# Kernel optimization log

Hardware: AMD Instinct MI355X
Metric: run time of the kernel (lower is better)

## Reference

```python
import jax, jax.numpy as jnp
import numpy as np

G, D, W, IN_CH, OUT_CH = 16, 8, 64, 3, 4
SKIPS = (4,)
B, N = 1, 65536


def _ilayers():
    il = [IN_CH] + [W] * (D - 1)
    for i in SKIPS:
        il[i + 1] += IN_CH
    return il


def setup_inputs() -> dict:
    key = jax.random.key(0)
    ks = jax.random.split(key, 2 * D + 3)
    inp = {"x": jax.random.normal(ks[0], (B, G, N, IN_CH), jnp.float32)}
    il = _ilayers()
    ki = 1
    for i, ci in enumerate(il):
        s = 1.0 / np.sqrt(ci)
        inp[f"w{i}"] = jax.random.uniform(ks[ki], (G, W, ci), jnp.float32, -s, s); ki += 1
        inp[f"b{i}"] = jax.random.uniform(ks[ki], (G, W), jnp.float32, -s, s); ki += 1
    s = 1.0 / np.sqrt(W)
    inp["w_out"] = jax.random.uniform(ks[ki], (G, OUT_CH, W), jnp.float32, -s, s)
    inp["b_out"] = jax.random.uniform(ks[ki + 1], (G, OUT_CH), jnp.float32, -s, s)
    return inp


def _plinear(h, w, b):
    # per-group linear: h [B,G,N,Ci], w [G,Co,Ci], b [G,Co] -> [B,G,N,Co]
    return jnp.einsum('bgnc,goc->bgno', h, w) + b[None, :, None, :]


def reference(x, w0, b0, w1, b1, w2, b2, w3, b3, w4, b4, w5, b5, w6, b6, w7, b7, w_out, b_out):
    ws = [w0, w1, w2, w3, w4, w5, w6, w7]
    bs = [b0, b1, b2, b3, b4, b5, b6, b7]
    h = x
    for i in range(D):
        h = jax.nn.relu(_plinear(h, ws[i], bs[i]))
        if i in SKIPS:
            # parallel_concat([x, h], G): per-group channel concat
            h = jnp.concatenate([x, h], axis=-1)
    out = _plinear(h, w_out, b_out)  # identity final activation
    return out, h
```

## Files before the change

### kernel.cpp

```cpp
#include <hip/hip_runtime.h>
#include <hip/hip_bf16.h>


#define NG 16
#define NPTS 65536
#define NT 4

typedef __attribute__((ext_vector_type(8))) short bf16x8;
typedef __attribute__((ext_vector_type(4))) float f32x4;
typedef __attribute__((ext_vector_type(4))) int i32x4;

#define SLOT_ELEMS 4096
#define GROUP_ELEMS (10 * SLOT_ELEMS)
#define WBUF_ELEMS (NG * GROUP_ELEMS)

__device__ __forceinline__ unsigned short f2bf(float f) {
  unsigned u = __builtin_bit_cast(unsigned, f);
  u += 0x7FFFu + ((u >> 16) & 1u);
  return (unsigned short)(u >> 16);
}
__device__ __forceinline__ float bf2f(unsigned short h) {
  return __builtin_bit_cast(float, ((unsigned)h) << 16);
}
__device__ __forceinline__ unsigned pkbf(float a, float b) {
  __hip_bfloat162 t = __float22bfloat162_rn(make_float2(a, b));
  unsigned u;
  __builtin_memcpy(&u, &t, 4);
  return u;
}
__device__ __forceinline__ float lo2f(unsigned u) { return __builtin_bit_cast(float, u << 16); }
__device__ __forceinline__ float hi2f(unsigned u) { return __builtin_bit_cast(float, u & 0xFFFF0000u); }
__device__ __forceinline__ bf16x8 pack4(unsigned a, unsigned b, unsigned cc, unsigned d) {
  i32x4 t;
  t[0] = (int)a; t[1] = (int)b; t[2] = (int)cc; t[3] = (int)d;
  return __builtin_bit_cast(bf16x8, t);
}

__device__ __forceinline__ int sig(int k) {
  int kt = k >> 5, qq = (k >> 3) & 3, j = k & 7;
  return (kt * 2 + (j >> 2)) * 16 + qq * 4 + (j & 3);
}

__global__ __launch_bounds__(256) void prep_weights(
    const float* __restrict__ w0, const float* __restrict__ w1,
    const float* __restrict__ w2, const float* __restrict__ w3,
    const float* __restrict__ w4, const float* __restrict__ w5,
    const float* __restrict__ w6, const float* __restrict__ w7,
    const float* __restrict__ w_out,
    unsigned short* __restrict__ whi, unsigned short* __restrict__ wlo) {
  int idx = blockIdx.x * 256 + threadIdx.x;
  if (idx >= WBUF_ELEMS) return;
  int g = idx / GROUP_ELEMS;
  int rem = idx - g * GROUP_ELEMS;
  int slot = rem / SLOT_ELEMS;
  int rc = rem - slot * SLOT_ELEMS;
  int row = rc >> 6, col = rc & 63;
  int sc = sig(col);
  float v = 0.0f;
  switch (slot) {
    case 0: if (col < 3) v = w0[g * 192 + row * 3 + col]; break;
    case 1: v = w1[g * 4096 + row * 64 + sc]; break;
    case 2: v = w2[g * 4096 + row * 64 + sc]; break;
    case 3: v = w3[g * 4096 + row * 64 + sc]; break;
    case 4: v = w4[g * 4096 + row * 64 + sc]; break;
    case 5: v = w5[g * 4288 + row * 67 + 3 + sc]; break;
    case 6: v = w6[g * 4096 + row * 64 + sc]; break;
    case 7: v = w7[g * 4096 + row * 64 + sc]; break;
    case 8: if (col < 3) v = w5[g * 4288 + row * 67 + col]; break;
    case 9: if (row < 4) v = w_out[g * 256 + row * 64 + sc]; break;
  }
  unsigned short h = f2bf(v);
  whi[idx] = h;
  wlo[idx] = f2bf(v - bf2f(h));
}

__device__ __forceinline__ void zeroC(f32x4 (&C)[4][NT]) {
#pragma unroll
  for (int mt = 0; mt < 4; ++mt)
#pragma unroll
    for (int nt = 0; nt < NT; ++nt) {
      f32x4 z = {0.f, 0.f, 0.f, 0.f};
      C[mt][nt] = z;
    }
}

__device__ __forceinline__ void cvt_all(f32x4 (&C)[4][NT], const float4* __restrict__ bias4,
                                        int q, bf16x8 (&Bh)[NT][2], bf16x8 (&Bl)[NT][2]) {
  float4 bs[4];
#pragma unroll
  for (int mt = 0; mt < 4; ++mt) bs[mt] = bias4[mt * 4 + q];
#pragma unroll
  for (int nt = 0; nt < NT; ++nt) {
    float v[4][4];
#pragma unroll
    for (int mt = 0; mt < 4; ++mt) {
      f32x4 cc = C[mt][nt];
      float t0 = fmaxf(cc[0] + bs[mt].x, 0.f);
      float t1 = fmaxf(cc[1] + bs[mt].y, 0.f);
      float t2 = fmaxf(cc[2] + bs[mt].z, 0.f);
      float t3 = fmaxf(cc[3] + bs[mt].w, 0.f);
      v[mt][0] = t0; v[mt][1] = t1; v[mt][2] = t2; v[mt][3] = t3;
      cc[0] = t0; cc[1] = t1; cc[2] = t2; cc[3] = t3;
      C[mt][nt] = cc;
    }
#pragma unroll
    for (int kt = 0; kt < 2; ++kt) {
      const float* a = v[2 * kt];
      const float* b = v[2 * kt + 1];
      unsigned u0 = pkbf(a[0], a[1]), u1 = pkbf(a[2], a[3]);
      unsigned u2 = pkbf(b[0], b[1]), u3 = pkbf(b[2], b[3]);
      Bh[nt][kt] = pack4(u0, u1, u2, u3);
      unsigned l0 = pkbf(a[0] - lo2f(u0), a[1] - hi2f(u0));
      unsigned l1 = pkbf(a[2] - lo2f(u1), a[3] - hi2f(u1));
      unsigned l2 = pkbf(b[0] - lo2f(u2), b[1] - hi2f(u2));
      unsigned l3 = pkbf(b[2] - lo2f(u3), b[3] - hi2f(u3));
      Bl[nt][kt] = pack4(l0, l1, l2, l3);
    }
  }
}

__device__ __forceinline__ void dense(const unsigned short* __restrict__ wh,
                                      const unsigned short* __restrict__ wl,
                                      int q, int c,
                                      const bf16x8 (&Bh)[NT][2], const bf16x8 (&Bl)[NT][2],
                                      f32x4 (&C)[4][NT]) {
  bf16x8 Ah[4][2];
#pragma unroll
  for (int mt = 0; mt < 4; ++mt)
#pragma unroll
    for (int kt = 0; kt < 2; ++kt)
      Ah[mt][kt] = *(const bf16x8*)(wh + (mt * 16 + c) * 64 + kt * 32 + q * 8);

#pragma unroll
  for (int mt = 0; mt < 4; ++mt)
#pragma unroll
    for (int kt = 0; kt < 2; ++kt) {
#pragma unroll
      for (int nt = 0; nt < NT; ++nt)
        C[mt][nt] = __builtin_amdgcn_mfma_f32_16x16x32_bf16(Ah[mt][kt], Bh[nt][kt], C[mt][nt], 0, 0, 0);
#pragma unroll
      for (int nt = 0; nt < NT; ++nt)
        C[mt][nt] = __builtin_amdgcn_mfma_f32_16x16x32_bf16(Ah[mt][kt], Bl[nt][kt], C[mt][nt], 0, 0, 0);
    }

#pragma unroll
  for (int mt = 0; mt < 4; ++mt)
#pragma unroll
    for (int kt = 0; kt < 2; ++kt) {
      bf16x8 Al = *(const bf16x8*)(wl + (mt * 16 + c) * 64 + kt * 32 + q * 8);
#pragma unroll
      for (int nt = 0; nt < NT; ++nt)
        C[mt][nt] = __builtin_amdgcn_mfma_f32_16x16x32_bf16(Al, Bh[nt][kt], C[mt][nt], 0, 0, 0);
    }
}

__device__ __forceinline__ void xpart(const unsigned short* __restrict__ wh,
                                      const unsigned short* __restrict__ wl,
                                      int q, int c, const float (&xr)[NT][3], f32x4 (&C)[4][NT]) {
  bf16x8 Bxh[NT], Bxl[NT];
#pragma unroll
  for (int nt = 0; nt < NT; ++nt) {
    unsigned u0 = 0, u1 = 0, l0 = 0, l1 = 0;
    if (q == 0) {
      u0 = pkbf(xr[nt][0], xr[nt][1]);
      u1 = pkbf(xr[nt][2], 0.f);
      l0 = pkbf(xr[nt][0] - lo2f(u0), xr[nt][1] - hi2f(u0));
      l1 = pkbf(xr[nt][2] - lo2f(u1), 0.f);
    }
    Bxh[nt] = pack4(u0, u1, 0, 0);
    Bxl[nt] = pack4(l0, l1, 0, 0);
  }
#pragma unroll
  for (int mt = 0; mt < 4; ++mt) {
    bf16x8 Ah = *(const bf16x8*)(wh + (mt * 16 + c) * 64 + q * 8);
    bf16x8 Al = *(const bf16x8*)(wl + (mt * 16 + c) * 64 + q * 8);
#pragma unroll
    for (int nt = 0; nt < NT; ++nt) {
      C[mt][nt] = __builtin_amdgcn_mfma_f32_16x16x32_bf16(Ah, Bxh[nt], C[mt][nt], 0, 0, 0);
      C[mt][nt] = __builtin_amdgcn_mfma_f32_16x16x32_bf16(Ah, Bxl[nt], C[mt][nt], 0, 0, 0);
      C[mt][nt] = __builtin_amdgcn_mfma_f32_16x16x32_bf16(Al, Bxh[nt], C[mt][nt], 0, 0, 0);
    }
  }
}

__global__ __launch_bounds__(256, 2) void mlp_mfma_kernel(
    const float* __restrict__ x,
    const float* __restrict__ b0, const float* __restrict__ b1,
    const float* __restrict__ b2, const float* __restrict__ b3,
    const float* __restrict__ b4, const float* __restrict__ b5,
    const float* __restrict__ b6, const float* __restrict__ b7,
    const float* __restrict__ b_out,
    const unsigned short* __restrict__ whi, const unsigned short* __restrict__ wlo,
    float* __restrict__ out, float* __restrict__ hfinal) {
  const int g = blockIdx.y;
  const int lane = threadIdx.x & 63;
  const int wv = threadIdx.x >> 6;
  const int q = lane >> 4;
  const int c = lane & 15;
  const int n0 = blockIdx.x * (64 * 4) + wv * 64;

  const unsigned short* wgh = whi + (size_t)g * GROUP_ELEMS;
  const unsigned short* wgl = wlo + (size_t)g * GROUP_ELEMS;

  float xr[NT][3];
#pragma unroll
  for (int nt = 0; nt < NT; ++nt) {
    const float* xp = x + ((size_t)g * NPTS + n0 + nt * 16 + c) * 3;
    xr[nt][0] = xp[0]; xr[nt][1] = xp[1]; xr[nt][2] = xp[2];
  }

  f32x4 C[4][NT];
  bf16x8 Bh[NT][2], Bl[NT][2];

  zeroC(C);
  xpart(wgh + 0 * SLOT_ELEMS, wgl + 0 * SLOT_ELEMS, q, c, xr, C);
  cvt_all(C, (const float4*)(b0 + g * 64), q, Bh, Bl);

  zeroC(C); dense(wgh + 1 * SLOT_ELEMS, wgl + 1 * SLOT_ELEMS, q, c, Bh, Bl, C);
  cvt_all(C, (const float4*)(b1 + g * 64), q, Bh, Bl);
  zeroC(C); dense(wgh + 2 * SLOT_ELEMS, wgl + 2 * SLOT_ELEMS, q, c, Bh, Bl, C);
  cvt_all(C, (const float4*)(b2 + g * 64), q, Bh, Bl);
  zeroC(C); dense(wgh + 3 * SLOT_ELEMS, wgl + 3 * SLOT_ELEMS, q, c, Bh, Bl, C);
  cvt_all(C, (const float4*)(b3 + g * 64), q, Bh, Bl);
  zeroC(C); dense(wgh + 4 * SLOT_ELEMS, wgl + 4 * SLOT_ELEMS, q, c, Bh, Bl, C);
  cvt_all(C, (const float4*)(b4 + g * 64), q, Bh, Bl);

  zeroC(C);
  xpart(wgh + 8 * SLOT_ELEMS, wgl + 8 * SLOT_ELEMS, q, c, xr, C);
  dense(wgh + 5 * SLOT_ELEMS, wgl + 5 * SLOT_ELEMS, q, c, Bh, Bl, C);
  cvt_all(C, (const float4*)(b5 + g * 64), q, Bh, Bl);

  zeroC(C); dense(wgh + 6 * SLOT_ELEMS, wgl + 6 * SLOT_ELEMS, q, c, Bh, Bl, C);
  cvt_all(C, (const float4*)(b6 + g * 64), q, Bh, Bl);
  zeroC(C); dense(wgh + 7 * SLOT_ELEMS, wgl + 7 * SLOT_ELEMS, q, c, Bh, Bl, C);
  cvt_all(C, (const float4*)(b7 + g * 64), q, Bh, Bl);

#pragma unroll
  for (int mt = 0; mt < 4; ++mt) {
#pragma unroll
    for (int nt = 0; nt < NT; ++nt) {
      size_t ptg = (size_t)g * NPTS + n0 + nt * 16 + c;
      f32x4 v = C[mt][nt];
      *(float4*)(hfinal + ptg * 64 + mt * 16 + q * 4) = make_float4(v[0], v[1], v[2], v[3]);
    }
  }

  f32x4 Co[NT];
#pragma unroll
  for (int nt = 0; nt < NT; ++nt) {
    f32x4 z = {0.f, 0.f, 0.f, 0.f};
    Co[nt] = z;
  }
#pragma unroll
  for (int kt = 0; kt < 2; ++kt) {
    bf16x8 Ah = *(const bf16x8*)(wgh + 9 * SLOT_ELEMS + c * 64 + kt * 32 + q * 8);
    bf16x8 Al = *(const bf16x8*)(wgl + 9 * SLOT_ELEMS + c * 64 + kt * 32 + q * 8);
#pragma unroll
    for (int nt = 0; nt < NT; ++nt) {
      Co[nt] = __builtin_amdgcn_mfma_f32_16x16x32_bf16(Ah, Bh[nt][kt], Co[nt], 0, 0, 0);
      Co[nt] = __builtin_amdgcn_mfma_f32_16x16x32_bf16(Ah, Bl[nt][kt], Co[nt], 0, 0, 0);
      Co[nt] = __builtin_amdgcn_mfma_f32_16x16x32_bf16(Al, Bh[nt][kt], Co[nt], 0, 0, 0);
    }
  }
  if (q == 0) {
    float4 bo = *(const float4*)(b_out + g * 4);
#pragma unroll
    for (int nt = 0; nt < NT; ++nt) {
      size_t ptg = (size_t)g * NPTS + n0 + nt * 16 + c;
      *(float4*)(out + ptg * 4) =
          make_float4(Co[nt][0] + bo.x, Co[nt][1] + bo.y, Co[nt][2] + bo.z, Co[nt][3] + bo.w);
    }
  }
}

extern "C" void kernel_launch(void* const* d_in, const int* in_sizes, int n_in,
                              void* d_out, int out_size, void* d_ws, size_t ws_size,
                              hipStream_t stream) {
  const float* x  = (const float*)d_in[0];
  const float* w0 = (const float*)d_in[1];  const float* b0 = (const float*)d_in[2];
  const float* w1 = (const float*)d_in[3];  const float* b1 = (const float*)d_in[4];
  const float* w2 = (const float*)d_in[5];  const float* b2 = (const float*)d_in[6];
  const float* w3 = (const float*)d_in[7];  const float* b3 = (const float*)d_in[8];
  const float* w4 = (const float*)d_in[9];  const float* b4 = (const float*)d_in[10];
  const float* w5 = (const float*)d_in[11]; const float* b5 = (const float*)d_in[12];
  const float* w6 = (const float*)d_in[13]; const float* b6 = (const float*)d_in[14];
  const float* w7 = (const float*)d_in[15]; const float* b7 = (const float*)d_in[16];
  const float* w_out = (const float*)d_in[17];
  const float* b_out = (const float*)d_in[18];

  float* out    = (float*)d_out;
  float* hfinal = (float*)d_out + (size_t)NG * NPTS * 4;

  unsigned short* whi = (unsigned short*)d_ws;
  unsigned short* wlo = whi + WBUF_ELEMS;

  prep_weights<<<dim3((WBUF_ELEMS + 255) / 256), dim3(256), 0, stream>>>(
      w0, w1, w2, w3, w4, w5, w6, w7, w_out, whi, wlo);

  mlp_mfma_kernel<<<dim3(NPTS / 256, NG), dim3(256), 0, stream>>>(
      x, b0, b1, b2, b3, b4, b5, b6, b7, b_out, whi, wlo, out, hfinal);
}
```

Measured before the change: 582.5 us.

## Prefetch next layer's weights across layers, halve point tile, raise occupancy

Cuts the per-wave point tile from 64 to 32 points (NT 4→2), doubles the grid, and raises launch_bounds to three blocks per CU to increase occupancy. It also software-pipelines the weight fragment loads: the next layer's hi weights are loaded at the end of each dense step, and the lo weights are loaded mid-computation. MFMA sections are wrapped in s_setprio raises. The ReLU result is written back into C only for the final layer. Smaller tiles reuse each weight fragment across fewer points, while the larger grid and register prefetch aim to hide load latency.

```diff
diff --git a/kernel.cpp b/kernel.cpp
--- a/kernel.cpp
+++ b/kernel.cpp
@@ -4,7 +4,7 @@
 
 #define NG 16
 #define NPTS 65536
-#define NT 4
+#define NT 2
 
 typedef __attribute__((ext_vector_type(8))) short bf16x8;
 typedef __attribute__((ext_vector_type(4))) float f32x4;
@@ -13,6 +13,8 @@
 #define SLOT_ELEMS 4096
 #define GROUP_ELEMS (10 * SLOT_ELEMS)
 #define WBUF_ELEMS (NG * GROUP_ELEMS)
+
+#define MFMA16(a, b, c) __builtin_amdgcn_mfma_f32_16x16x32_bf16((a), (b), (c), 0, 0, 0)
 
 __device__ __forceinline__ unsigned short f2bf(float f) {
   unsigned u = __builtin_bit_cast(unsigned, f);
@@ -84,6 +86,7 @@
     }
 }
 
+template <bool KEEPC>
 __device__ __forceinline__ void cvt_all(f32x4 (&C)[4][NT], const float4* __restrict__ bias4,
                                         int q, bf16x8 (&Bh)[NT][2], bf16x8 (&Bl)[NT][2]) {
   float4 bs[4];
@@ -100,8 +103,10 @@
       float t2 = fmaxf(cc[2] + bs[mt].z, 0.f);
       float t3 = fmaxf(cc[3] + bs[mt].w, 0.f);
       v[mt][0] = t0; v[mt][1] = t1; v[mt][2] = t2; v[mt][3] = t3;
-      cc[0] = t0; cc[1] = t1; cc[2] = t2; cc[3] = t3;
-      C[mt][nt] = cc;
+      if (KEEPC) {
+        cc[0] = t0; cc[1] = t1; cc[2] = t2; cc[3] = t3;
+        C[mt][nt] = cc;
+      }
     }
 #pragma unroll
     for (int kt = 0; kt < 2; ++kt) {
@@ -119,39 +124,55 @@
   }
 }
 
-__device__ __forceinline__ void dense(const unsigned short* __restrict__ wh,
-                                      const unsigned short* __restrict__ wl,
-                                      int q, int c,
-                                      const bf16x8 (&Bh)[NT][2], const bf16x8 (&Bl)[NT][2],
-                                      f32x4 (&C)[4][NT]) {
-  bf16x8 Ah[4][2];
-#pragma unroll
-  for (int mt = 0; mt < 4; ++mt)
-#pragma unroll
-    for (int kt = 0; kt < 2; ++kt)
-      Ah[mt][kt] = *(const bf16x8*)(wh + (mt * 16 + c) * 64 + kt * 32 + q * 8);
-
-#pragma unroll
-  for (int mt = 0; mt < 4; ++mt)
-#pragma unroll
-    for (int kt = 0; kt < 2; ++kt) {
+__device__ __forceinline__ void dense_pipe(const unsigned short* __restrict__ wl,
+                                           const unsigned short* __restrict__ wh_next,
+                                           int q, int c,
+                                           const bf16x8 (&Bh)[NT][2], const bf16x8 (&Bl)[NT][2],
+                                           f32x4 (&C)[4][NT], bf16x8 (&Ah)[4][2]) {
+  __builtin_amdgcn_s_setprio(1);
+#pragma unroll
+  for (int mt = 0; mt < 2; ++mt)
+#pragma unroll
+    for (int kt = 0; kt < 2; ++kt)
+#pragma unroll
+      for (int nt = 0; nt < NT; ++nt) {
+        C[mt][nt] = MFMA16(Ah[mt][kt], Bh[nt][kt], C[mt][nt]);
+        C[mt][nt] = MFMA16(Ah[mt][kt], Bl[nt][kt], C[mt][nt]);
+      }
+  __builtin_amdgcn_s_setprio(0);
+
+  bf16x8 Al[4][2];
+#pragma unroll
+  for (int mt = 0; mt < 4; ++mt)
+#pragma unroll
+    for (int kt = 0; kt < 2; ++kt)
+      Al[mt][kt] = *(const bf16x8*)(wl + (mt * 16 + c) * 64 + kt * 32 + q * 8);
+
+  __builtin_amdgcn_s_setprio(1);
+#pragma unroll
+  for (int mt = 2; mt < 4; ++mt)
+#pragma unroll
+    for (int kt = 0; kt < 2; ++kt)
+#pragma unroll
+      for (int nt = 0; nt < NT; ++nt) {
+        C[mt][nt] = MFMA16(Ah[mt][kt], Bh[nt][kt], C[mt][nt]);
+        C[mt][nt] = MFMA16(Ah[mt][kt], Bl[nt][kt], C[mt][nt]);
+      }
+
+#pragma unroll
+  for (int mt = 0; mt < 4; ++mt)
+#pragma unroll
+    for (int kt = 0; kt < 2; ++kt)
 #pragma unroll
       for (int nt = 0; nt < NT; ++nt)
-        C[mt][nt] = __builtin_amdgcn_mfma_f32_16x16x32_bf16(Ah[mt][kt], Bh[nt][kt], C[mt][nt], 0, 0, 0);
-#pragma unroll
-      for (int nt = 0; nt < NT; ++nt)
-        C[mt][nt] = __builtin_amdgcn_mfma_f32_16x16x32_bf16(Ah[mt][kt], Bl[nt][kt], C[mt][nt], 0, 0, 0);
-    }
-
-#pragma unroll
-  for (int mt = 0; mt < 4; ++mt)
-#pragma unroll
-    for (int kt = 0; kt < 2; ++kt) {
-      bf16x8 Al = *(const bf16x8*)(wl + (mt * 16 + c) * 64 + kt * 32 + q * 8);
-#pragma unroll
-      for (int nt = 0; nt < NT; ++nt)
-        C[mt][nt] = __builtin_amdgcn_mfma_f32_16x16x32_bf16(Al, Bh[nt][kt], C[mt][nt], 0, 0, 0);
-    }
+        C[mt][nt] = MFMA16(Al[mt][kt], Bh[nt][kt], C[mt][nt]);
+  __builtin_amdgcn_s_setprio(0);
+
+#pragma unroll
+  for (int mt = 0; mt < 4; ++mt)
+#pragma unroll
+    for (int kt = 0; kt < 2; ++kt)
+      Ah[mt][kt] = *(const bf16x8*)(wh_next + (mt * 16 + c) * 64 + kt * 32 + q * 8);
 }
 
 __device__ __forceinline__ void xpart(const unsigned short* __restrict__ wh,
@@ -176,14 +197,14 @@
     bf16x8 Al = *(const bf16x8*)(wl + (mt * 16 + c) * 64 + q * 8);
 #pragma unroll
     for (int nt = 0; nt < NT; ++nt) {
-      C[mt][nt] = __builtin_amdgcn_mfma_f32_16x16x32_bf16(Ah, Bxh[nt], C[mt][nt], 0, 0, 0);
-      C[mt][nt] = __builtin_amdgcn_mfma_f32_16x16x32_bf16(Ah, Bxl[nt], C[mt][nt], 0, 0, 0);
-      C[mt][nt] = __builtin_amdgcn_mfma_f32_16x16x32_bf16(Al, Bxh[nt], C[mt][nt], 0, 0, 0);
-    }
-  }
-}
-
-__global__ __launch_bounds__(256, 2) void mlp_mfma_kernel(
+      C[mt][nt] = MFMA16(Ah, Bxh[nt], C[mt][nt]);
+      C[mt][nt] = MFMA16(Ah, Bxl[nt], C[mt][nt]);
+      C[mt][nt] = MFMA16(Al, Bxh[nt], C[mt][nt]);
+    }
+  }
+}
+
+__global__ __launch_bounds__(256, 3) void mlp_mfma_kernel(
     const float* __restrict__ x,
     const float* __restrict__ b0, const float* __restrict__ b1,
     const float* __restrict__ b2, const float* __restrict__ b3,
@@ -197,10 +218,17 @@
   const int wv = threadIdx.x >> 6;
   const int q = lane >> 4;
   const int c = lane & 15;
-  const int n0 = blockIdx.x * (64 * 4) + wv * 64;
+  const int n0 = blockIdx.x * (32 * 4) + wv * 32;
 
   const unsigned short* wgh = whi + (size_t)g * GROUP_ELEMS;
   const unsigned short* wgl = wlo + (size_t)g * GROUP_ELEMS;
+
+  bf16x8 Ah[4][2];
+#pragma unroll
+  for (int mt = 0; mt < 4; ++mt)
+#pragma unroll
+    for (int kt = 0; kt < 2; ++kt)
+      Ah[mt][kt] = *(const bf16x8*)(wgh + 1 * SLOT_ELEMS + (mt * 16 + c) * 64 + kt * 32 + q * 8);
 
   float xr[NT][3];
 #pragma unroll
@@ -214,26 +242,26 @@
 
   zeroC(C);
   xpart(wgh + 0 * SLOT_ELEMS, wgl + 0 * SLOT_ELEMS, q, c, xr, C);
-  cvt_all(C, (const float4*)(b0 + g * 64), q, Bh, Bl);
-
-  zeroC(C); dense(wgh + 1 * SLOT_ELEMS, wgl + 1 * SLOT_ELEMS, q, c, Bh, Bl, C);
-  cvt_all(C, (const float4*)(b1 + g * 64), q, Bh, Bl);
-  zeroC(C); dense(wgh + 2 * SLOT_ELEMS, wgl + 2 * SLOT_ELEMS, q, c, Bh, Bl, C);
-  cvt_all(C, (const float4*)(b2 + g * 64), q, Bh, Bl);
-  zeroC(C); dense(wgh + 3 * SLOT_ELEMS, wgl + 3 * SLOT_ELEMS, q, c, Bh, Bl, C);
-  cvt_all(C, (const float4*)(b3 + g * 64), q, Bh, Bl);
-  zeroC(C); dense(wgh + 4 * SLOT_ELEMS, wgl + 4 * SLOT_ELEMS, q, c, Bh, Bl, C);
-  cvt_all(C, (const float4*)(b4 + g * 64), q, Bh, Bl);
+  cvt_all<false>(C, (const float4*)(b0 + g * 64), q, Bh, Bl);
+
+  zeroC(C); dense_pipe(wgl + 1 * SLOT_ELEMS, wgh + 2 * SLOT_ELEMS, q, c, Bh, Bl, C, Ah);
+  cvt_all<false>(C, (const float4*)(b1 + g * 64), q, Bh, Bl);
+  zeroC(C); dense_pipe(wgl + 2 * SLOT_ELEMS, wgh + 3 * SLOT_ELEMS, q, c, Bh, Bl, C, Ah);
+  cvt_all<false>(C, (const float4*)(b2 + g * 64), q, Bh, Bl);
+  zeroC(C); dense_pipe(wgl + 3 * SLOT_ELEMS, wgh + 4 * SLOT_ELEMS, q, c, Bh, Bl, C, Ah);
+  cvt_all<false>(C, (const float4*)(b3 + g * 64), q, Bh, Bl);
+  zeroC(C); dense_pipe(wgl + 4 * SLOT_ELEMS, wgh + 5 * SLOT_ELEMS, q, c, Bh, Bl, C, Ah);
+  cvt_all<false>(C, (const float4*)(b4 + g * 64), q, Bh, Bl);
 
   zeroC(C);
   xpart(wgh + 8 * SLOT_ELEMS, wgl + 8 * SLOT_ELEMS, q, c, xr, C);
-  dense(wgh + 5 * SLOT_ELEMS, wgl + 5 * SLOT_ELEMS, q, c, Bh, Bl, C);
-  cvt_all(C, (const float4*)(b5 + g * 64), q, Bh, Bl);
-
-  zeroC(C); dense(wgh + 6 * SLOT_ELEMS, wgl + 6 * SLOT_ELEMS, q, c, Bh, Bl, C);
-  cvt_all(C, (const float4*)(b6 + g * 64), q, Bh, Bl);
-  zeroC(C); dense(wgh + 7 * SLOT_ELEMS, wgl + 7 * SLOT_ELEMS, q, c, Bh, Bl, C);
-  cvt_all(C, (const float4*)(b7 + g * 64), q, Bh, Bl);
+  dense_pipe(wgl + 5 * SLOT_ELEMS, wgh + 6 * SLOT_ELEMS, q, c, Bh, Bl, C, Ah);
+  cvt_all<false>(C, (const float4*)(b5 + g * 64), q, Bh, Bl);
+
+  zeroC(C); dense_pipe(wgl + 6 * SLOT_ELEMS, wgh + 7 * SLOT_ELEMS, q, c, Bh, Bl, C, Ah);
+  cvt_all<false>(C, (const float4*)(b6 + g * 64), q, Bh, Bl);
+  zeroC(C); dense_pipe(wgl + 7 * SLOT_ELEMS, wgh + 9 * SLOT_ELEMS, q, c, Bh, Bl, C, Ah);
+  cvt_all<true>(C, (const float4*)(b7 + g * 64), q, Bh, Bl);
 
 #pragma unroll
   for (int mt = 0; mt < 4; ++mt) {
@@ -253,13 +281,12 @@
   }
 #pragma unroll
   for (int kt = 0; kt < 2; ++kt) {
-    bf16x8 Ah = *(const bf16x8*)(wgh + 9 * SLOT_ELEMS + c * 64 + kt * 32 + q * 8);
     bf16x8 Al = *(const bf16x8*)(wgl + 9 * SLOT_ELEMS + c * 64 + kt * 32 + q * 8);
 #pragma unroll
     for (int nt = 0; nt < NT; ++nt) {
-      Co[nt] = __builtin_amdgcn_mfma_f32_16x16x32_bf16(Ah, Bh[nt][kt], Co[nt], 0, 0, 0);
-      Co[nt] = __builtin_amdgcn_mfma_f32_16x16x32_bf16(Ah, Bl[nt][kt], Co[nt], 0, 0, 0);
-      Co[nt] = __builtin_amdgcn_mfma_f32_16x16x32_bf16(Al, Bh[nt][kt], Co[nt], 0, 0, 0);
+      Co[nt] = MFMA16(Ah[0][kt], Bh[nt][kt], Co[nt]);
+      Co[nt] = MFMA16(Ah[0][kt], Bl[nt][kt], Co[nt]);
+      Co[nt] = MFMA16(Al, Bh[nt][kt], Co[nt]);
     }
   }
   if (q == 0) {
@@ -297,6 +324,6 @@
   prep_weights<<<dim3((WBUF_ELEMS + 255) / 256), dim3(256), 0, stream>>>(
       w0, w1, w2, w3, w4, w5, w6, w7, w_out, whi, wlo);
 
-  mlp_mfma_kernel<<<dim3(NPTS / 256, NG), dim3(256), 0, stream>>>(
+  mlp_mfma_kernel<<<dim3(NPTS / 128, NG), dim3(256), 0, stream>>>(
       x, b0, b1, b2, b3, b4, b5, b6, b7, b_out, whi, wlo, out, hfinal);
 }
```

Result: slower. 779.0 us (+33.7%).
